# Performance work log

Hardware: AMD Instinct MI355X
Metric: run time of the kernel (lower is better)

The kernel has to match this reference:

```python
import jax, jax.numpy as jnp
import numpy as np

N = 100_000
E = 1_600_000
HEADS = 4
HID = 16
OUT = 64
NEG_SLOPE_ATT = 0.2   # PyG GATConv attention leaky_relu
NEG_SLOPE_ACT = 0.01  # F.leaky_relu default between layers


def setup_inputs() -> dict:
    key = jax.random.key(0)
    ks = jax.random.split(key, 16)
    x = jax.random.normal(ks[0], (N, 2), dtype=jnp.float32)
    edge_index = jax.random.randint(ks[1], (2, E), 0, N, dtype=jnp.int64)
    def glorot(k, shape):
        fan = sum(shape[-2:]) if len(shape) >= 2 else shape[-1] * 2
        return jax.random.normal(k, shape, dtype=jnp.float32) * jnp.sqrt(2.0 / fan)
    # layer 0: 2 -> 16 per head, 4 heads, concat
    W0 = glorot(ks[2], (2, HEADS * HID))
    as0 = glorot(ks[3], (HEADS, HID))
    ad0 = glorot(ks[4], (HEADS, HID))
    b0 = jnp.zeros((HEADS * HID,), jnp.float32)
    # layer 1: 64 -> 16 per head, 4 heads, concat
    W1 = glorot(ks[5], (HEADS * HID, HEADS * HID))
    as1 = glorot(ks[6], (HEADS, HID))
    ad1 = glorot(ks[7], (HEADS, HID))
    b1 = jnp.zeros((HEADS * HID,), jnp.float32)
    # layer 2: 64 -> 64, 1 head, no concat
    W2 = glorot(ks[8], (HEADS * HID, OUT))
    as2 = glorot(ks[9], (1, OUT))
    ad2 = glorot(ks[10], (1, OUT))
    b2 = jnp.zeros((OUT,), jnp.float32)
    return {"x": x, "edge_index": edge_index,
            "W0": W0, "as0": as0, "ad0": ad0, "b0": b0,
            "W1": W1, "as1": as1, "ad1": ad1, "b1": b1,
            "W2": W2, "as2": as2, "ad2": ad2, "b2": b2}


def gat_conv(x, src, dst, W, a_src, a_dst, b, heads, out_ch, concat):
    n = x.shape[0]
    h = (x @ W).reshape(n, heads, out_ch)                 # [N,H,C]
    alpha_s = jnp.sum(h * a_src[None], axis=-1)           # [N,H]
    alpha_d = jnp.sum(h * a_dst[None], axis=-1)           # [N,H]
    logits = jax.nn.leaky_relu(alpha_s[src] + alpha_d[dst], NEG_SLOPE_ATT)  # [E,H]
    # segment softmax over edges grouped by target node (self-loops guarantee nonempty)
    m = jax.ops.segment_max(logits, dst, num_segments=n)
    e = jnp.exp(logits - m[dst])
    s = jax.ops.segment_sum(e, dst, num_segments=n)
    alpha = e / s[dst]                                    # [E,H]
    msg = h[src] * alpha[:, :, None]                      # [E,H,C]
    out = jax.ops.segment_sum(msg, dst, num_segments=n)   # [N,H,C]
    out = out.reshape(n, heads * out_ch) if concat else out.mean(axis=1)
    return out + b


def reference(x, edge_index, W0, as0, ad0, b0, W1, as1, ad1, b1, W2, as2, ad2, b2):
    n = x.shape[0]
    loops = jnp.arange(n, dtype=edge_index.dtype)
    src = jnp.concatenate([edge_index[0], loops])  # PyG add_self_loops=True
    dst = jnp.concatenate([edge_index[1], loops])
    h = gat_conv(x, src, dst, W0, as0, ad0, b0, HEADS, HID, True)
    h = jax.nn.leaky_relu(h, NEG_SLOPE_ACT)  # dropout p=0.5 -> identity in eval
    h = gat_conv(h, src, dst, W1, as1, ad1, b1, HEADS, HID, True)
    h = jax.nn.leaky_relu(h, NEG_SLOPE_ACT)
    return gat_conv(h, src, dst, W2, as2, ad2, b2, 1, OUT, False)
```

## Files before the change

### kernel.cpp

```cpp
#include <hip/hip_runtime.h>
#include <hip/hip_bf16.h>


#define LRELU(x, a) fmaxf((x), (a) * (x))
typedef unsigned int u32;
typedef unsigned short u16;

#define NBUCKET 256
#define CAP_A 12288
#define OVCAP 65536

__device__ __forceinline__ float bf2f(u16 v) { return __uint_as_float(((u32)v) << 16); }
__device__ __forceinline__ u16 f2bf(float f) {
    u32 u = __float_as_uint(f);
    return (u16)((u + 0x7FFF + ((u >> 16) & 1)) >> 16);
}

__global__ __launch_bounds__(1024) void k_detect(const int* __restrict__ eraw, int e,
                                                 int* __restrict__ flag) {
    int i = threadIdx.x;
    long long step = (long long)e / 1024;
    if (step == 0) step = 1;
    long long pos = 2LL * (i * step) + 1;
    if (pos < 2LL * e && eraw[pos] != 0) atomicExch(flag, 1);
}

__global__ __launch_bounds__(64) void k_prep(const float* __restrict__ W2,
                                             const float* __restrict__ as2,
                                             const float* __restrict__ ad2,
                                             float* __restrict__ va, float* __restrict__ vd) {
    int k = threadIdx.x;
    float sa = 0.f, sd = 0.f;
    for (int j = 0; j < 64; j++) {
        float w = W2[k * 64 + j];
        sa += w * as2[j];
        sd += w * ad2[j];
    }
    va[k] = sa;
    vd[k] = sd;
}

#define ACHUNK 2048
__global__ __launch_bounds__(256) void k_passA(const int* __restrict__ eraw, int e, int etot,
                                               const int* __restrict__ flag, int n,
                                               int2* __restrict__ pairs, int* __restrict__ gcnt,
                                               int2* __restrict__ ovp, int* __restrict__ ovcnt) {
    __shared__ int bcnt[NBUCKET];
    if (threadIdx.x < NBUCKET) bcnt[threadIdx.x] = 0;
    __syncthreads();
    const int base = blockIdx.x * ACHUNK;
    const bool i64 = (*flag == 0);
    int s_[8], d_[8], b_[8];
    #pragma unroll
    for (int j = 0; j < 8; j++) {
        int i = base + j * 256 + threadIdx.x;
        if (i < etot) {
            int s, d;
            if (i < e) {
                if (i64) { s = eraw[2 * i]; d = eraw[2 * (e + i)]; }
                else     { s = eraw[i];     d = eraw[e + i]; }
            } else { s = i - e; d = i - e; }
            s_[j] = s; d_[j] = d;
            int b = (int)(((long long)d * NBUCKET) / n);
            b_[j] = b;
            atomicAdd(&bcnt[b], 1);
        } else b_[j] = -1;
    }
    __syncthreads();
    if (threadIdx.x < NBUCKET) {
        int c = bcnt[threadIdx.x];
        bcnt[threadIdx.x] = (c > 0) ? atomicAdd(&gcnt[threadIdx.x], c) : 0;
    }
    __syncthreads();
    #pragma unroll
    for (int j = 0; j < 8; j++) {
        if (b_[j] >= 0) {
            int slot = atomicAdd(&bcnt[b_[j]], 1);
            if (slot < CAP_A) {
                pairs[(size_t)b_[j] * CAP_A + slot] = make_int2(s_[j], d_[j]);
            } else {
                int ov = atomicAdd(ovcnt, 1);
                if (ov < OVCAP) ovp[ov] = make_int2(s_[j], d_[j]);
            }
        }
    }
}

__global__ __launch_bounds__(256) void k_passB(const int2* __restrict__ pairs,
                                               const int* __restrict__ gcnt,
                                               const int2* __restrict__ ovp,
                                               const int* __restrict__ ovcnt, int n, int etot,
                                               int* __restrict__ rowstart,
                                               int* __restrict__ csr) {
    __shared__ int lcsr[CAP_A];
    __shared__ int lscan[512];
    __shared__ int lcur[512];
    __shared__ int gscan[NBUCKET];
    const int b = blockIdx.x;
    const int tid = threadIdx.x;
    const int node_lo = (int)(((long long)b * n + NBUCKET - 1) / NBUCKET);
    const int node_hi = (int)(((long long)(b + 1) * n + NBUCKET - 1) / NBUCKET);
    const int nodes = node_hi - node_lo;
    const int cnt_total = gcnt[b];
    const int stored = min(cnt_total, CAP_A);
    const int nov = min(*ovcnt, OVCAP);

    gscan[tid] = gcnt[tid];
    __syncthreads();
    #pragma unroll
    for (int o = 1; o < NBUCKET; o <<= 1) {
        int v = (tid >= o) ? gscan[tid - o] : 0;
        __syncthreads();
        gscan[tid] += v;
        __syncthreads();
    }
    const int bucket_base = (b == 0) ? 0 : gscan[b - 1];

    lscan[tid] = 0; lscan[tid + 256] = 0;
    __syncthreads();
    for (int i = tid; i < stored; i += 256) {
        int d = pairs[(size_t)b * CAP_A + i].y;
        atomicAdd(&lscan[d - node_lo], 1);
    }
    for (int i = tid; i < nov; i += 256) {
        int d = ovp[i].y;
        if (d >= node_lo && d < node_hi) atomicAdd(&lscan[d - node_lo], 1);
    }
    __syncthreads();
    #pragma unroll
    for (int o = 1; o < 512; o <<= 1) {
        int i0 = tid, i1 = tid + 256;
        int v0 = (i0 >= o) ? lscan[i0 - o] : 0;
        int v1 = (i1 >= o) ? lscan[i1 - o] : 0;
        __syncthreads();
        lscan[i0] += v0; lscan[i1] += v1;
        __syncthreads();
    }
    #pragma unroll
    for (int t = 0; t < 2; t++) {
        int j = tid + t * 256;
        int excl = (j == 0) ? 0 : lscan[j - 1];
        lcur[j] = excl;
        if (j < nodes) rowstart[node_lo + j] = bucket_base + excl;
    }
    if (b == NBUCKET - 1 && tid == 0) rowstart[n] = etot;
    __syncthreads();
    for (int i = tid; i < stored; i += 256) {
        int2 p = pairs[(size_t)b * CAP_A + i];
        int slot = atomicAdd(&lcur[p.y - node_lo], 1);
        lcsr[slot] = p.x;
    }
    for (int i = tid; i < nov; i += 256) {
        int2 p = ovp[i];
        if (p.y >= node_lo && p.y < node_hi) {
            int slot = atomicAdd(&lcur[p.y - node_lo], 1);
            lcsr[slot] = p.x;
        }
    }
    __syncthreads();
    for (int i = tid; i < cnt_total; i += 256) csr[bucket_base + i] = lcsr[i];
}

__global__ __launch_bounds__(256) void k_feat0(const float* __restrict__ Xin,
                                               const float* __restrict__ W,
                                               const float* __restrict__ Asrc,
                                               const float* __restrict__ Adst,
                                               u16* __restrict__ Hb, float* __restrict__ asn,
                                               float* __restrict__ adn, int n) {
    const int wv = threadIdx.x >> 6, ln = threadIdx.x & 63;
    const float w0 = W[ln], w1 = W[64 + ln];
    const float a_s = Asrc[ln], a_d = Adst[ln];
    for (int node = blockIdx.x * 4 + wv; node < n; node += gridDim.x * 4) {
        float x0 = Xin[node * 2 + 0], x1 = Xin[node * 2 + 1];
        float acc = fmaf(x1, w1, x0 * w0);
        float ts = acc * a_s, td = acc * a_d;
        #pragma unroll
        for (int o = 1; o < 16; o <<= 1) {
            ts += __shfl_xor(ts, o, 16);
            td += __shfl_xor(td, o, 16);
        }
        Hb[node * 64 + ln] = f2bf(acc);
        if ((ln & 15) == 0) {
            asn[node * 4 + (ln >> 4)] = ts;
            adn[node * 4 + (ln >> 4)] = td;
        }
    }
}

__global__ __launch_bounds__(256) void k_feat64(const float* __restrict__ Xin,
                                                const float* __restrict__ W,
                                                const float* __restrict__ Asrc,
                                                const float* __restrict__ Adst,
                                                u16* __restrict__ Hb, float* __restrict__ asn,
                                                float* __restrict__ adn, int n) {
    __shared__ float Ws[64 * 64];
    __shared__ __align__(16) float Xs[4][256];
    for (int i = threadIdx.x; i < 64 * 64; i += 256) Ws[i] = W[i];
    __syncthreads();
    const int wv = threadIdx.x >> 6, ln = threadIdx.x & 63;
    const float a_s = Asrc[ln], a_d = Adst[ln];
    const int r = ln >> 4;
    const int c4 = (ln & 15) * 4;
    for (int g0 = blockIdx.x * 16 + wv * 4; g0 < n; g0 += gridDim.x * 16) {
        int node_r = g0 + r;
        float4 xq = (node_r < n) ? *(const float4*)&Xin[(size_t)node_r * 64 + c4]
                                 : make_float4(0.f, 0.f, 0.f, 0.f);
        Xs[wv][(c4 + 0) * 4 + r] = xq.x;
        Xs[wv][(c4 + 1) * 4 + r] = xq.y;
        Xs[wv][(c4 + 2) * 4 + r] = xq.z;
        Xs[wv][(c4 + 3) * 4 + r] = xq.w;
        float acc0 = 0.f, acc1 = 0.f, acc2 = 0.f, acc3 = 0.f;
        #pragma unroll 8
        for (int k = 0; k < 64; k++) {
            float w = Ws[k * 64 + ln];
            float4 xk = *(const float4*)&Xs[wv][k * 4];
            acc0 = fmaf(xk.x, w, acc0);
            acc1 = fmaf(xk.y, w, acc1);
            acc2 = fmaf(xk.z, w, acc2);
            acc3 = fmaf(xk.w, w, acc3);
        }
        #pragma unroll
        for (int j = 0; j < 4; j++) {
            int node = g0 + j;
            if (node >= n) break;
            float acc = (j == 0) ? acc0 : (j == 1) ? acc1 : (j == 2) ? acc2 : acc3;
            float ts = acc * a_s, td = acc * a_d;
            #pragma unroll
            for (int o = 1; o < 16; o <<= 1) {
                ts += __shfl_xor(ts, o, 16);
                td += __shfl_xor(td, o, 16);
            }
            Hb[(size_t)node * 64 + ln] = f2bf(acc);
            if ((ln & 15) == 0) {
                asn[node * 4 + (ln >> 4)] = ts;
                adn[node * 4 + (ln >> 4)] = td;
            }
        }
    }
}

template <int HEADS, int OUTMODE>
__global__ __launch_bounds__(256) void k_edge(const u16* __restrict__ Hb,
                                              const float* __restrict__ asn,
                                              const float* __restrict__ adn,
                                              const int* __restrict__ rowstart,
                                              const int* __restrict__ csr,
                                              const float* __restrict__ bias,
                                              float4* __restrict__ Outf,
                                              u16* __restrict__ Outb,
                                              const float* __restrict__ va,
                                              const float* __restrict__ vd,
                                              float* __restrict__ asn2,
                                              float* __restrict__ adn2, int n) {
    const int wv = threadIdx.x >> 6, ln = threadIdx.x & 63;
    const int node = blockIdx.x * 4 + wv;
    if (node >= n) return;
    const int g = ln >> 3, q = ln & 7;
    const int head = (HEADS == 4) ? (q >> 1) : 0;
    const int start = rowstart[node], end = rowstart[node + 1];
    const float adme = adn[node * HEADS + head];

    float a0 = 0.f, a1 = 0.f, a2 = 0.f, a3 = 0.f, a4 = 0.f, a5 = 0.f, a6 = 0.f, a7 = 0.f;
    float sw = 0.f;
    for (int eg = start + g; eg < end; eg += 8) {
        int s = csr[eg];
        float l = LRELU(asn[s * HEADS + head] + adme, 0.2f);
        float w = __expf(l);
        sw += w;
        uint4 hv = ((const uint4*)Hb)[s * 8 + q];
        a0 = fmaf(w, bf2f((u16)(hv.x & 0xffff)), a0);
        a1 = fmaf(w, bf2f((u16)(hv.x >> 16)), a1);
        a2 = fmaf(w, bf2f((u16)(hv.y & 0xffff)), a2);
        a3 = fmaf(w, bf2f((u16)(hv.y >> 16)), a3);
        a4 = fmaf(w, bf2f((u16)(hv.z & 0xffff)), a4);
        a5 = fmaf(w, bf2f((u16)(hv.z >> 16)), a5);
        a6 = fmaf(w, bf2f((u16)(hv.w & 0xffff)), a6);
        a7 = fmaf(w, bf2f((u16)(hv.w >> 16)), a7);
    }
    #pragma unroll
    for (int o = 8; o < 64; o <<= 1) {
        a0 += __shfl_xor(a0, o); a1 += __shfl_xor(a1, o);
        a2 += __shfl_xor(a2, o); a3 += __shfl_xor(a3, o);
        a4 += __shfl_xor(a4, o); a5 += __shfl_xor(a5, o);
        a6 += __shfl_xor(a6, o); a7 += __shfl_xor(a7, o);
        sw += __shfl_xor(sw, o);
    }
    if (ln < 8) {
        const float inv = 1.0f / sw;
        float r0 = a0 * inv, r1 = a1 * inv, r2 = a2 * inv, r3 = a3 * inv;
        float r4 = a4 * inv, r5 = a5 * inv, r6 = a6 * inv, r7 = a7 * inv;
        if constexpr (OUTMODE != 2) {
            const float4 bA = ((const float4*)bias)[2 * q];
            const float4 bB = ((const float4*)bias)[2 * q + 1];
            r0 = LRELU(r0 + bA.x, 0.01f); r1 = LRELU(r1 + bA.y, 0.01f);
            r2 = LRELU(r2 + bA.z, 0.01f); r3 = LRELU(r3 + bA.w, 0.01f);
            r4 = LRELU(r4 + bB.x, 0.01f); r5 = LRELU(r5 + bB.y, 0.01f);
            r6 = LRELU(r6 + bB.z, 0.01f); r7 = LRELU(r7 + bB.w, 0.01f);
        }
        if constexpr (OUTMODE == 1) {
            uint4 pb;
            pb.x = (u32)f2bf(r0) | ((u32)f2bf(r1) << 16);
            pb.y = (u32)f2bf(r2) | ((u32)f2bf(r3) << 16);
            pb.z = (u32)f2bf(r4) | ((u32)f2bf(r5) << 16);
            pb.w = (u32)f2bf(r6) | ((u32)f2bf(r7) << 16);
            ((uint4*)Outb)[node * 8 + q] = pb;
            const float4 vA = ((const float4*)va)[2 * q];
            const float4 vB = ((const float4*)va)[2 * q + 1];
            const float4 dA = ((const float4*)vd)[2 * q];
            const float4 dB = ((const float4*)vd)[2 * q + 1];
            float ts = r0 * vA.x + r1 * vA.y + r2 * vA.z + r3 * vA.w +
                       r4 * vB.x + r5 * vB.y + r6 * vB.z + r7 * vB.w;
            float td = r0 * dA.x + r1 * dA.y + r2 * dA.z + r3 * dA.w +
                       r4 * dB.x + r5 * dB.y + r6 * dB.z + r7 * dB.w;
            ts += __shfl_xor(ts, 1, 8); td += __shfl_xor(td, 1, 8);
            ts += __shfl_xor(ts, 2, 8); td += __shfl_xor(td, 2, 8);
            ts += __shfl_xor(ts, 4, 8); td += __shfl_xor(td, 4, 8);
            if (ln == 0) { asn2[node] = ts; adn2[node] = td; }
        } else {
            float4 oA = make_float4(r0, r1, r2, r3);
            float4 oB = make_float4(r4, r5, r6, r7);
            Outf[node * 16 + 2 * q] = oA;
            Outf[node * 16 + 2 * q + 1] = oB;
        }
    }
}

__global__ __launch_bounds__(256) void k_out(const float* __restrict__ Agg,
                                             const float* __restrict__ W2,
                                             const float* __restrict__ b2,
                                             float* __restrict__ Out, int n) {
    __shared__ float Ws[64 * 64];
    __shared__ __align__(16) float Xs[4][256];
    for (int i = threadIdx.x; i < 64 * 64; i += 256) Ws[i] = W2[i];
    __syncthreads();
    const int wv = threadIdx.x >> 6, ln = threadIdx.x & 63;
    const float bb = b2[ln];
    const int r = ln >> 4;
    const int c4 = (ln & 15) * 4;
    for (int g0 = blockIdx.x * 16 + wv * 4; g0 < n; g0 += gridDim.x * 16) {
        int node_r = g0 + r;
        float4 xq = (node_r < n) ? *(const float4*)&Agg[(size_t)node_r * 64 + c4]
                                 : make_float4(0.f, 0.f, 0.f, 0.f);
        Xs[wv][(c4 + 0) * 4 + r] = xq.x;
        Xs[wv][(c4 + 1) * 4 + r] = xq.y;
        Xs[wv][(c4 + 2) * 4 + r] = xq.z;
        Xs[wv][(c4 + 3) * 4 + r] = xq.w;
        float acc0 = 0.f, acc1 = 0.f, acc2 = 0.f, acc3 = 0.f;
        #pragma unroll 8
        for (int k = 0; k < 64; k++) {
            float w = Ws[k * 64 + ln];
            float4 xk = *(const float4*)&Xs[wv][k * 4];
            acc0 = fmaf(xk.x, w, acc0);
            acc1 = fmaf(xk.y, w, acc1);
            acc2 = fmaf(xk.z, w, acc2);
            acc3 = fmaf(xk.w, w, acc3);
        }
        #pragma unroll
        for (int j = 0; j < 4; j++) {
            int node = g0 + j;
            if (node >= n) break;
            float acc = (j == 0) ? acc0 : (j == 1) ? acc1 : (j == 2) ? acc2 : acc3;
            Out[(size_t)node * 64 + ln] = acc + bb;
        }
    }
}

extern "C" void kernel_launch(void* const* d_in, const int* in_sizes, int n_in, void* d_out,
                              int out_size, void* d_ws, size_t ws_size, hipStream_t stream) {
    const float* x = (const float*)d_in[0];
    const int* eraw = (const int*)d_in[1];
    const float* W0 = (const float*)d_in[2];
    const float* as0 = (const float*)d_in[3];
    const float* ad0 = (const float*)d_in[4];
    const float* b0 = (const float*)d_in[5];
    const float* W1 = (const float*)d_in[6];
    const float* as1 = (const float*)d_in[7];
    const float* ad1 = (const float*)d_in[8];
    const float* b1 = (const float*)d_in[9];
    const float* W2 = (const float*)d_in[10];
    const float* as2 = (const float*)d_in[11];
    const float* ad2 = (const float*)d_in[12];
    const float* b2 = (const float*)d_in[13];

    const int n = in_sizes[0] / 2;
    const int e = in_sizes[1] / 2;
    const int etot = e + n;

    char* wp = (char*)d_ws;
    size_t off = 0;
    auto take = [&](size_t bytes) -> void* {
        void* p = wp + off;
        off = (off + bytes + 255) & ~(size_t)255;
        return p;
    };
    size_t hsz = (size_t)n * 64 * 2;
    size_t psz = (size_t)NBUCKET * CAP_A * 8;
    size_t usz = 2 * hsz > psz ? 2 * hsz : psz;
    char* ubase   = (char*)take(usz);
    u16* Hbf      = (u16*)ubase;
    u16* Xb2      = (u16*)(ubase + hsz);
    int2* pairs   = (int2*)ubase;
    float* asn    = (float*)take((size_t)n * 4 * 4);
    float* adn    = (float*)take((size_t)n * 4 * 4);
    float* asn2   = (float*)take((size_t)n * 4);
    float* adn2   = (float*)take((size_t)n * 4);
    int* rowstart = (int*)take((size_t)(n + 1) * 4);
    int* gcnt     = (int*)take(NBUCKET * 4);
    int* flag     = (int*)take(256);
    int* ovcnt    = flag + 1;
    float* va     = (float*)take(64 * 4);
    float* vd     = (float*)take(64 * 4);
    int2* ovp     = (int2*)take((size_t)OVCAP * 8);
    int* csr      = (int*)take((size_t)etot * 4);
    (void)ws_size;

    hipMemsetAsync(gcnt, 0, NBUCKET * 4, stream);
    hipMemsetAsync(flag, 0, 256, stream);

    k_detect<<<1, 1024, 0, stream>>>(eraw, e, flag);
    k_prep<<<1, 64, 0, stream>>>(W2, as2, ad2, va, vd);
    k_passA<<<(etot + ACHUNK - 1) / ACHUNK, 256, 0, stream>>>(eraw, e, etot, flag, n, pairs,
                                                              gcnt, ovp, ovcnt);
    k_passB<<<NBUCKET, 256, 0, stream>>>(pairs, gcnt, ovp, ovcnt, n, etot, rowstart, csr);

    const int nodeBlocks4 = (n + 3) / 4;
    const int gemmBlocks = 2048;
    float* Xact = (float*)d_out;

    k_feat0<<<nodeBlocks4, 256, 0, stream>>>(x, W0, as0, ad0, Hbf, asn, adn, n);
    k_edge<4, 0><<<nodeBlocks4, 256, 0, stream>>>(Hbf, asn, adn, rowstart, csr, b0,
                                                  (float4*)Xact, nullptr, nullptr, nullptr,
                                                  nullptr, nullptr, n);
    k_feat64<<<gemmBlocks, 256, 0, stream>>>(Xact, W1, as1, ad1, Hbf, asn, adn, n);
    k_edge<4, 1><<<nodeBlocks4, 256, 0, stream>>>(Hbf, asn, adn, rowstart, csr, b1,
                                                  nullptr, Xb2, va, vd, asn2, adn2, n);
    k_edge<1, 2><<<nodeBlocks4, 256, 0, stream>>>(Xb2, asn2, adn2, rowstart, csr, nullptr,
                                                  (float4*)Xact, nullptr, nullptr, nullptr,
                                                  nullptr, nullptr, n);
    k_out<<<gemmBlocks, 256, 0, stream>>>(Xact, W2, b2, (float*)d_out, n);
}
```

Before: 309.3 us.

## Pack bucket edge keys into 32 bits, prefetch CSR via shuffle, merge init kernels

Three separate changes. The bucketing pass now stores each edge as one 32-bit key (source index plus local destination offset shifted by 18) instead of an int2 pair, halving scratch traffic between passA and passB. The edge aggregation kernels preload up to 64 CSR neighbour indices per wave in one coalesced load, distribute them with shuffles, and accumulate into packed float2 vectors. The detect and prep kernels are merged into one launch. The key packing assumes source ids fit in 18 bits and local destination offsets fit in the remaining 14 bits.

```diff
diff --git a/kernel.cpp b/kernel.cpp
--- a/kernel.cpp
+++ b/kernel.cpp
@@ -16,41 +16,41 @@
     return (u16)((u + 0x7FFF + ((u >> 16) & 1)) >> 16);
 }
 
-__global__ __launch_bounds__(1024) void k_detect(const int* __restrict__ eraw, int e,
-                                                 int* __restrict__ flag) {
+__global__ __launch_bounds__(1024) void k_init(const int* __restrict__ eraw, int e,
+                                               int* __restrict__ flag,
+                                               const float* __restrict__ W2,
+                                               const float* __restrict__ as2,
+                                               const float* __restrict__ ad2,
+                                               float* __restrict__ va, float* __restrict__ vd) {
     int i = threadIdx.x;
     long long step = (long long)e / 1024;
     if (step == 0) step = 1;
     long long pos = 2LL * (i * step) + 1;
     if (pos < 2LL * e && eraw[pos] != 0) atomicExch(flag, 1);
-}
-
-__global__ __launch_bounds__(64) void k_prep(const float* __restrict__ W2,
-                                             const float* __restrict__ as2,
-                                             const float* __restrict__ ad2,
-                                             float* __restrict__ va, float* __restrict__ vd) {
-    int k = threadIdx.x;
-    float sa = 0.f, sd = 0.f;
-    for (int j = 0; j < 64; j++) {
-        float w = W2[k * 64 + j];
-        sa += w * as2[j];
-        sd += w * ad2[j];
-    }
-    va[k] = sa;
-    vd[k] = sd;
+    if (i < 64) {
+        float sa = 0.f, sd = 0.f;
+        for (int j = 0; j < 64; j++) {
+            float w = W2[i * 64 + j];
+            sa += w * as2[j];
+            sd += w * ad2[j];
+        }
+        va[i] = sa;
+        vd[i] = sd;
+    }
 }
 
 #define ACHUNK 2048
 __global__ __launch_bounds__(256) void k_passA(const int* __restrict__ eraw, int e, int etot,
                                                const int* __restrict__ flag, int n,
-                                               int2* __restrict__ pairs, int* __restrict__ gcnt,
+                                               u32* __restrict__ keys, int* __restrict__ gcnt,
                                                int2* __restrict__ ovp, int* __restrict__ ovcnt) {
     __shared__ int bcnt[NBUCKET];
-    if (threadIdx.x < NBUCKET) bcnt[threadIdx.x] = 0;
+    bcnt[threadIdx.x] = 0;
     __syncthreads();
     const int base = blockIdx.x * ACHUNK;
     const bool i64 = (*flag == 0);
     int s_[8], d_[8], b_[8];
+    u32 key_[8];
     #pragma unroll
     for (int j = 0; j < 8; j++) {
         int i = base + j * 256 + threadIdx.x;
@@ -62,12 +62,14 @@
             } else { s = i - e; d = i - e; }
             s_[j] = s; d_[j] = d;
             int b = (int)(((long long)d * NBUCKET) / n);
+            int node_lo_b = (int)(((long long)b * n + NBUCKET - 1) / NBUCKET);
             b_[j] = b;
+            key_[j] = (u32)s | ((u32)(d - node_lo_b) << 18);
             atomicAdd(&bcnt[b], 1);
         } else b_[j] = -1;
     }
     __syncthreads();
-    if (threadIdx.x < NBUCKET) {
+    {
         int c = bcnt[threadIdx.x];
         bcnt[threadIdx.x] = (c > 0) ? atomicAdd(&gcnt[threadIdx.x], c) : 0;
     }
@@ -77,7 +79,7 @@
         if (b_[j] >= 0) {
             int slot = atomicAdd(&bcnt[b_[j]], 1);
             if (slot < CAP_A) {
-                pairs[(size_t)b_[j] * CAP_A + slot] = make_int2(s_[j], d_[j]);
+                keys[(size_t)b_[j] * CAP_A + slot] = key_[j];
             } else {
                 int ov = atomicAdd(ovcnt, 1);
                 if (ov < OVCAP) ovp[ov] = make_int2(s_[j], d_[j]);
@@ -86,7 +88,7 @@
     }
 }
 
-__global__ __launch_bounds__(256) void k_passB(const int2* __restrict__ pairs,
+__global__ __launch_bounds__(256) void k_passB(const u32* __restrict__ keys,
                                                const int* __restrict__ gcnt,
                                                const int2* __restrict__ ovp,
                                                const int* __restrict__ ovcnt, int n, int etot,
@@ -119,8 +121,8 @@
     lscan[tid] = 0; lscan[tid + 256] = 0;
     __syncthreads();
     for (int i = tid; i < stored; i += 256) {
-        int d = pairs[(size_t)b * CAP_A + i].y;
-        atomicAdd(&lscan[d - node_lo], 1);
+        int dloc = keys[(size_t)b * CAP_A + i] >> 18;
+        atomicAdd(&lscan[dloc], 1);
     }
     for (int i = tid; i < nov; i += 256) {
         int d = ovp[i].y;
@@ -146,9 +148,9 @@
     if (b == NBUCKET - 1 && tid == 0) rowstart[n] = etot;
     __syncthreads();
     for (int i = tid; i < stored; i += 256) {
-        int2 p = pairs[(size_t)b * CAP_A + i];
-        int slot = atomicAdd(&lcur[p.y - node_lo], 1);
-        lcsr[slot] = p.x;
+        u32 k = keys[(size_t)b * CAP_A + i];
+        int slot = atomicAdd(&lcur[k >> 18], 1);
+        lcsr[slot] = (int)(k & 0x3FFFFu);
     }
     for (int i = tid; i < nov; i += 256) {
         int2 p = ovp[i];
@@ -239,6 +241,29 @@
     }
 }
 
+#define EDGE_BODY(SRC)                                                        \
+    {                                                                         \
+        int s_e = (SRC);                                                      \
+        float l = LRELU(asn[s_e * HEADS + head] + adme, 0.2f);                \
+        float w = __expf(l);                                                  \
+        sw += w;                                                              \
+        uint4 hv = ((const uint4*)Hb)[s_e * 8 + q];                           \
+        v2f w2 = {w, w};                                                      \
+        v2f h;                                                                \
+        h.x = __uint_as_float(hv.x << 16);                                    \
+        h.y = __uint_as_float(hv.x & 0xffff0000u);                            \
+        p0 += w2 * h;                                                         \
+        h.x = __uint_as_float(hv.y << 16);                                    \
+        h.y = __uint_as_float(hv.y & 0xffff0000u);                            \
+        p1 += w2 * h;                                                         \
+        h.x = __uint_as_float(hv.z << 16);                                    \
+        h.y = __uint_as_float(hv.z & 0xffff0000u);                            \
+        p2 += w2 * h;                                                         \
+        h.x = __uint_as_float(hv.w << 16);                                    \
+        h.y = __uint_as_float(hv.w & 0xffff0000u);                            \
+        p3 += w2 * h;                                                         \
+    }
+
 template <int HEADS, int OUTMODE>
 __global__ __launch_bounds__(256) void k_edge(const u16* __restrict__ Hb,
                                               const float* __restrict__ asn,
@@ -252,43 +277,41 @@
                                               const float* __restrict__ vd,
                                               float* __restrict__ asn2,
                                               float* __restrict__ adn2, int n) {
+    typedef float v2f __attribute__((ext_vector_type(2)));
     const int wv = threadIdx.x >> 6, ln = threadIdx.x & 63;
     const int node = blockIdx.x * 4 + wv;
     if (node >= n) return;
     const int g = ln >> 3, q = ln & 7;
     const int head = (HEADS == 4) ? (q >> 1) : 0;
     const int start = rowstart[node], end = rowstart[node + 1];
+    const int deg = end - start;
     const float adme = adn[node * HEADS + head];
 
-    float a0 = 0.f, a1 = 0.f, a2 = 0.f, a3 = 0.f, a4 = 0.f, a5 = 0.f, a6 = 0.f, a7 = 0.f;
+    int sload = (ln < deg) ? csr[start + ln] : 0;
+
+    v2f p0 = {0.f, 0.f}, p1 = {0.f, 0.f}, p2 = {0.f, 0.f}, p3 = {0.f, 0.f};
     float sw = 0.f;
-    for (int eg = start + g; eg < end; eg += 8) {
-        int s = csr[eg];
-        float l = LRELU(asn[s * HEADS + head] + adme, 0.2f);
-        float w = __expf(l);
-        sw += w;
-        uint4 hv = ((const uint4*)Hb)[s * 8 + q];
-        a0 = fmaf(w, bf2f((u16)(hv.x & 0xffff)), a0);
-        a1 = fmaf(w, bf2f((u16)(hv.x >> 16)), a1);
-        a2 = fmaf(w, bf2f((u16)(hv.y & 0xffff)), a2);
-        a3 = fmaf(w, bf2f((u16)(hv.y >> 16)), a3);
-        a4 = fmaf(w, bf2f((u16)(hv.z & 0xffff)), a4);
-        a5 = fmaf(w, bf2f((u16)(hv.z >> 16)), a5);
-        a6 = fmaf(w, bf2f((u16)(hv.w & 0xffff)), a6);
-        a7 = fmaf(w, bf2f((u16)(hv.w >> 16)), a7);
-    }
+    const int mainE = deg < 64 ? deg : 64;
+    const int T = (mainE + 7) >> 3;
+    for (int t = 0; t < T; t++) {
+        int i = g + 8 * t;
+        int s = __shfl(sload, i);
+        if (i < mainE) EDGE_BODY(s)
+    }
+    for (int eg = start + 64 + g; eg < end; eg += 8) EDGE_BODY(csr[eg])
+
     #pragma unroll
     for (int o = 8; o < 64; o <<= 1) {
-        a0 += __shfl_xor(a0, o); a1 += __shfl_xor(a1, o);
-        a2 += __shfl_xor(a2, o); a3 += __shfl_xor(a3, o);
-        a4 += __shfl_xor(a4, o); a5 += __shfl_xor(a5, o);
-        a6 += __shfl_xor(a6, o); a7 += __shfl_xor(a7, o);
+        p0.x += __shfl_xor(p0.x, o); p0.y += __shfl_xor(p0.y, o);
+        p1.x += __shfl_xor(p1.x, o); p1.y += __shfl_xor(p1.y, o);
+        p2.x += __shfl_xor(p2.x, o); p2.y += __shfl_xor(p2.y, o);
+        p3.x += __shfl_xor(p3.x, o); p3.y += __shfl_xor(p3.y, o);
         sw += __shfl_xor(sw, o);
     }
     if (ln < 8) {
         const float inv = 1.0f / sw;
-        float r0 = a0 * inv, r1 = a1 * inv, r2 = a2 * inv, r3 = a3 * inv;
-        float r4 = a4 * inv, r5 = a5 * inv, r6 = a6 * inv, r7 = a7 * inv;
+        float r0 = p0.x * inv, r1 = p0.y * inv, r2 = p1.x * inv, r3 = p1.y * inv;
+        float r4 = p2.x * inv, r5 = p2.y * inv, r6 = p3.x * inv, r7 = p3.y * inv;
         if constexpr (OUTMODE != 2) {
             const float4 bA = ((const float4*)bias)[2 * q];
             const float4 bB = ((const float4*)bias)[2 * q + 1];
@@ -394,12 +417,12 @@
         return p;
     };
     size_t hsz = (size_t)n * 64 * 2;
-    size_t psz = (size_t)NBUCKET * CAP_A * 8;
+    size_t psz = (size_t)NBUCKET * CAP_A * 4;
     size_t usz = 2 * hsz > psz ? 2 * hsz : psz;
     char* ubase   = (char*)take(usz);
     u16* Hbf      = (u16*)ubase;
     u16* Xb2      = (u16*)(ubase + hsz);
-    int2* pairs   = (int2*)ubase;
+    u32* keys     = (u32*)ubase;
     float* asn    = (float*)take((size_t)n * 4 * 4);
     float* adn    = (float*)take((size_t)n * 4 * 4);
     float* asn2   = (float*)take((size_t)n * 4);
@@ -417,11 +440,10 @@
     hipMemsetAsync(gcnt, 0, NBUCKET * 4, stream);
     hipMemsetAsync(flag, 0, 256, stream);
 
-    k_detect<<<1, 1024, 0, stream>>>(eraw, e, flag);
-    k_prep<<<1, 64, 0, stream>>>(W2, as2, ad2, va, vd);
-    k_passA<<<(etot + ACHUNK - 1) / ACHUNK, 256, 0, stream>>>(eraw, e, etot, flag, n, pairs,
+    k_init<<<1, 1024, 0, stream>>>(eraw, e, flag, W2, as2, ad2, va, vd);
+    k_passA<<<(etot + ACHUNK - 1) / ACHUNK, 256, 0, stream>>>(eraw, e, etot, flag, n, keys,
                                                               gcnt, ovp, ovcnt);
-    k_passB<<<NBUCKET, 256, 0, stream>>>(pairs, gcnt, ovp, ovcnt, n, etot, rowstart, csr);
+    k_passB<<<NBUCKET, 256, 0, stream>>>(keys, gcnt, ovp, ovcnt, n, etot, rowstart, csr);
 
     const int nodeBlocks4 = (n + 3) / 4;
     const int gemmBlocks = 2048;
```

Result: faster. 290.0 us (-6.2%).
